# Kernel tuning notes

Measured on AMD Instinct MI355X. Metric: run time of the kernel, lower is better.

Reference implementation:

```python
import jax, jax.numpy as jnp
import numpy as np

B, H, D, S = 128, 32, 128, 64   # batch, num_head, size_per_head, seq_len
START_LEN = 32
SCALE = 0.125  # hard-coded in source (not 1/sqrt(D))


def setup_inputs() -> dict:
    key = jax.random.key(0)
    ks = jax.random.split(key, 7)
    w_std = 1.0 / np.sqrt(D)  # xavier-ish, keeps softmax well-conditioned
    return {
        "x": jax.random.normal(ks[0], (B, H, 1, D), dtype=jnp.float32),
        "k": jax.random.normal(ks[1], (B, H, S, D), dtype=jnp.float32),
        "v": jax.random.normal(ks[2], (B, H, S, D), dtype=jnp.float32),
        "weight_q": jax.random.normal(ks[3], (H, D, D), dtype=jnp.float32) * w_std,
        "weight_k": jax.random.normal(ks[4], (H, D, D), dtype=jnp.float32) * w_std,
        "weight_v": jax.random.normal(ks[5], (H, D, D), dtype=jnp.float32) * w_std,
        "weight_o": jax.random.normal(ks[6], (H, D, D), dtype=jnp.float32) * w_std,
    }


def reference(x, k, v, weight_q, weight_k, weight_v, weight_o):
    # scatters K/V into the cache at gen_id, then attends over the FULL cache
    # (including not-yet-written zero slots, exactly as the torch code does).
    def step(carry, gen_id):
        x, k, v = carry
        q = jnp.einsum('bhod,hde->bhoe', x, weight_q)          # [B,H,1,D]
        k_new = jnp.einsum('bhod,hde->bhe', x, weight_k)       # [B,H,D]
        v_new = jnp.einsum('bhod,hde->bhe', x, weight_v)
        k = jax.lax.dynamic_update_slice_in_dim(k, k_new[:, :, None, :], gen_id, axis=2)
        v = jax.lax.dynamic_update_slice_in_dim(v, v_new[:, :, None, :], gen_id, axis=2)
        attn = jnp.einsum('bhsd,bhod->bhos', k, q) * SCALE     # [B,H,1,S]
        attn = jax.nn.softmax(attn, axis=3)
        x = jnp.einsum('bhos,bhsd->bhod', attn, v)             # [B,H,1,D]
        x = jnp.einsum('bhod,hde->bhoe', x, weight_o)
        return (x, k, v), None

    (x, k, v), _ = jax.lax.scan(step, (x, k, v), jnp.arange(START_LEN, S))
    return (k, v, x)
```

## Files before the change

### kernel.cpp

```cpp
#include <hip/hip_runtime.h>
#include <math.h>

#define B 128
#define H 32
#define D 128
#define S 64
#define T0 32
#define SCALE 0.125f

#define NB 2
#define NT 512
#define KVS 132

#define OFF_KL 0
#define OFF_VL (OFF_KL + NB*S*KVS)
#define OFF_X2 (OFF_VL + NB*S*KVS)
#define OFF_QB (OFF_X2 + 256)
#define OFF_XO (OFF_QB + 256)
#define OFF_RED (OFF_XO + 256)
#define OFF_AT (OFF_RED + 4096)
#define LDS_FLOATS (OFF_AT + 128)
#define LDS_BYTES (LDS_FLOATS*4)

__global__ void __launch_bounds__(NT, 2)
attn_decode_kernel(const float* __restrict__ x_in,
                   const float* __restrict__ k_in,
                   const float* __restrict__ v_in,
                   const float* __restrict__ wq,
                   const float* __restrict__ wk,
                   const float* __restrict__ wv,
                   const float* __restrict__ wo,
                   float* __restrict__ out)
{
    extern __shared__ float smem[];
    float* Kl    = smem + OFF_KL;
    float* Vl    = smem + OFF_VL;
    float* x2    = smem + OFF_X2;
    float* qb    = smem + OFF_QB;
    float* xo2   = smem + OFF_XO;
    float* red   = smem + OFF_RED;
    float* attnp = smem + OFF_AT;

    const int tid = threadIdx.x;
    const int blk = (blockIdx.x & 7) * 256 + (blockIdx.x >> 3);
    const int h  = blk >> 6;
    const int b0 = (blk & 63) << 1;

    const int m  = tid >> 7;
    const int dq = (tid >> 5) & 3;
    const int cg = tid & 31;
    const int ds = tid >> 5;

    float4 w[32];
    if (m < 3) {
        const float* Wm = (m == 0 ? wq : (m == 1 ? wk : wv)) + h*D*D + (dq*32)*D + cg*4;
        #pragma unroll
        for (int i = 0; i < 32; ++i)
            w[i] = *reinterpret_cast<const float4*>(Wm + i*D);
    }
    float4 wob[8];
    {
        const float* Wo = wo + h*D*D + (ds*8)*D + cg*4;
        #pragma unroll
        for (int i = 0; i < 8; ++i)
            wob[i] = *reinterpret_cast<const float4*>(Wo + i*D);
    }

    for (int i = tid; i < NB*S*(D/4); i += NT) {
        int p = i >> 11, s = (i >> 5) & 63, g = i & 31;
        size_t base = (size_t)((b0+p)*H + h) * S * D;
        float4 k4 = reinterpret_cast<const float4*>(k_in + base)[s*32 + g];
        float4 v4 = reinterpret_cast<const float4*>(v_in + base)[s*32 + g];
        *reinterpret_cast<float4*>(&Kl[(p*S + s)*KVS + g*4]) = k4;
        *reinterpret_cast<float4*>(&Vl[(p*S + s)*KVS + g*4]) = v4;
    }
    if (tid < 256) {
        int p = tid >> 7, d = tid & 127;
        x2[d*2 + p] = x_in[(size_t)((b0+p)*H + h)*D + d];
    }
    __syncthreads();

    for (int t = T0; t < S; ++t) {
        if (m < 3) {
            float4 a0 = {0,0,0,0}, a1 = {0,0,0,0};
            #pragma unroll
            for (int i = 0; i < 32; ++i) {
                float2 xd = *reinterpret_cast<const float2*>(&x2[(dq*32 + i)*2]);
                a0.x = fmaf(xd.x, w[i].x, a0.x); a0.y = fmaf(xd.x, w[i].y, a0.y);
                a0.z = fmaf(xd.x, w[i].z, a0.z); a0.w = fmaf(xd.x, w[i].w, a0.w);
                a1.x = fmaf(xd.y, w[i].x, a1.x); a1.y = fmaf(xd.y, w[i].y, a1.y);
                a1.z = fmaf(xd.y, w[i].z, a1.z); a1.w = fmaf(xd.y, w[i].w, a1.w);
            }
            *reinterpret_cast<float4*>(&red[((m*4 + dq)*2 + 0)*128 + cg*4]) = a0;
            *reinterpret_cast<float4*>(&red[((m*4 + dq)*2 + 1)*128 + cg*4]) = a1;
        }
        __syncthreads();
        for (int u = tid; u < 768; u += NT) {
            int mm = u >> 8, p = (u >> 7) & 1, col = u & 127;
            float sm = red[((mm*4+0)*2+p)*128+col] + red[((mm*4+1)*2+p)*128+col]
                     + red[((mm*4+2)*2+p)*128+col] + red[((mm*4+3)*2+p)*128+col];
            if (mm == 0)      qb[p*128 + col] = sm;
            else if (mm == 1) Kl[(p*S + t)*KVS + col] = sm;
            else              Vl[(p*S + t)*KVS + col] = sm;
        }
        __syncthreads();

        {
            int p = tid >> 8, dqq = (tid >> 6) & 3, s = tid & 63;
            const float* kr = &Kl[(p*S + s)*KVS + dqq*32];
            const float* qr = &qb[p*128 + dqq*32];
            float acc = 0.f;
            #pragma unroll
            for (int j = 0; j < 8; ++j) {
                float4 kk = *reinterpret_cast<const float4*>(kr + j*4);
                float4 qq = *reinterpret_cast<const float4*>(qr + j*4);
                acc = fmaf(kk.x, qq.x, fmaf(kk.y, qq.y, fmaf(kk.z, qq.z, fmaf(kk.w, qq.w, acc))));
            }
            red[(p*4 + dqq)*64 + s] = acc;
        }
        __syncthreads();

        if (tid < 128) {
            int p = tid >> 6, s = tid & 63;
            float a = (red[(p*4+0)*64+s] + red[(p*4+1)*64+s]
                     + red[(p*4+2)*64+s] + red[(p*4+3)*64+s]) * SCALE;
            float mx = a;
            #pragma unroll
            for (int k2 = 32; k2; k2 >>= 1) mx = fmaxf(mx, __shfl_xor(mx, k2));
            float e = expf(a - mx);
            float ssum = e;
            #pragma unroll
            for (int k2 = 32; k2; k2 >>= 1) ssum += __shfl_xor(ssum, k2);
            attnp[p*64 + s] = e / ssum;
        }
        __syncthreads();

        {
            int p = tid >> 8, sh = (tid >> 7) & 1, col = tid & 127;
            const float* pp = &attnp[p*64 + sh*32];
            float acc = 0.f;
            #pragma unroll
            for (int i = 0; i < 32; ++i)
                acc = fmaf(pp[i], Vl[(p*S + sh*32 + i)*KVS + col], acc);
            red[(p*2 + sh)*128 + col] = acc;
        }
        __syncthreads();
        if (tid < 256) {
            int p = tid >> 7, col = tid & 127;
            xo2[col*2 + p] = red[(p*2+0)*128+col] + red[(p*2+1)*128+col];
        }
        __syncthreads();

        {
            float4 a0 = {0,0,0,0}, a1 = {0,0,0,0};
            #pragma unroll
            for (int i = 0; i < 8; ++i) {
                float2 xd = *reinterpret_cast<const float2*>(&xo2[(ds*8 + i)*2]);
                a0.x = fmaf(xd.x, wob[i].x, a0.x); a0.y = fmaf(xd.x, wob[i].y, a0.y);
                a0.z = fmaf(xd.x, wob[i].z, a0.z); a0.w = fmaf(xd.x, wob[i].w, a0.w);
                a1.x = fmaf(xd.y, wob[i].x, a1.x); a1.y = fmaf(xd.y, wob[i].y, a1.y);
                a1.z = fmaf(xd.y, wob[i].z, a1.z); a1.w = fmaf(xd.y, wob[i].w, a1.w);
            }
            *reinterpret_cast<float4*>(&red[(ds*2 + 0)*128 + cg*4]) = a0;
            *reinterpret_cast<float4*>(&red[(ds*2 + 1)*128 + cg*4]) = a1;
        }
        __syncthreads();
        if (tid < 256) {
            int p = tid >> 7, col = tid & 127;
            float sm = 0.f;
            #pragma unroll
            for (int d16 = 0; d16 < 16; ++d16) sm += red[(d16*2 + p)*128 + col];
            x2[col*2 + p] = sm;
        }
        __syncthreads();
    }

    float* kout = out;
    float* vout = out + (size_t)B*H*S*D;
    float* xout = out + (size_t)2*B*H*S*D;
    for (int i = tid; i < NB*S*(D/4); i += NT) {
        int p = i >> 11, s = (i >> 5) & 63, g = i & 31;
        size_t base = (size_t)((b0+p)*H + h) * S * D;
        float4 k4 = *reinterpret_cast<const float4*>(&Kl[(p*S + s)*KVS + g*4]);
        float4 v4 = *reinterpret_cast<const float4*>(&Vl[(p*S + s)*KVS + g*4]);
        reinterpret_cast<float4*>(kout + base)[s*32 + g] = k4;
        reinterpret_cast<float4*>(vout + base)[s*32 + g] = v4;
    }
    if (tid < 256) {
        int p = tid >> 7, d = tid & 127;
        xout[(size_t)((b0+p)*H + h)*D + d] = x2[d*2 + p];
    }
}

extern "C" void kernel_launch(void* const* d_in, const int* in_sizes, int n_in,
                              void* d_out, int out_size, void* d_ws, size_t ws_size,
                              hipStream_t stream) {
    (void)in_sizes; (void)n_in; (void)out_size; (void)d_ws; (void)ws_size;
    const float* x  = (const float*)d_in[0];
    const float* k  = (const float*)d_in[1];
    const float* v  = (const float*)d_in[2];
    const float* wq = (const float*)d_in[3];
    const float* wk = (const float*)d_in[4];
    const float* wv = (const float*)d_in[5];
    const float* wo = (const float*)d_in[6];
    float* out = (float*)d_out;

    hipFuncSetAttribute(reinterpret_cast<const void*>(attn_decode_kernel),
                        hipFuncAttributeMaxDynamicSharedMemorySize, LDS_BYTES);

    dim3 grid(B*H/NB);
    dim3 block(NT);
    attn_decode_kernel<<<grid, block, LDS_BYTES, stream>>>(x, k, v, wq, wk, wv, wo, out);
}
```

Measured before the change: 1.211 ms.

## Replace LDS partial-sum reductions with wave shuffles and cut per-step barriers

Each decode step is re-partitioned so that every wave computes its slice of the Q/K/V projections, the QK scores, the softmax-weighted V sum and the output projection. Partial sums are reduced with cross-lane shuffles instead of an LDS staging buffer, which removes several reduction passes and roughly halves the __syncthreads barriers per step. All threads now keep scalar slices of all four weight matrices in registers, and the q, x and xo buffers use padded LDS layouts to avoid bank conflicts. In exchange it adds heavy register pressure (128 weight floats per thread), which could spill, plus extra shuffle traffic.

```diff
diff --git a/kernel.cpp b/kernel.cpp
--- a/kernel.cpp
+++ b/kernel.cpp
@@ -12,14 +12,17 @@
 #define NT 512
 #define KVS 132
 
+#define X2IDX(d,p) ((((d)>>5)*66) + (((d)&31)<<1) + (p))
+#define QPIDX(p,d) ((p)*160 + (((d)>>4)*20) + ((d)&15))
+
+#define SZ_KV  (NB*S*KVS)
 #define OFF_KL 0
-#define OFF_VL (OFF_KL + NB*S*KVS)
-#define OFF_X2 (OFF_VL + NB*S*KVS)
-#define OFF_QB (OFF_X2 + 256)
-#define OFF_XO (OFF_QB + 256)
-#define OFF_RED (OFF_XO + 256)
-#define OFF_AT (OFF_RED + 4096)
-#define LDS_FLOATS (OFF_AT + 128)
+#define OFF_VL (OFF_KL + SZ_KV)
+#define OFF_X2 (OFF_VL + SZ_KV)
+#define OFF_QP (OFF_X2 + 264)
+#define OFF_XO (OFF_QP + 320)
+#define OFF_SC (OFF_XO + 264)
+#define LDS_FLOATS (OFF_SC + 128)
 #define LDS_BYTES (LDS_FLOATS*4)
 
 __global__ void __launch_bounds__(NT, 2)
@@ -33,37 +36,37 @@
                    float* __restrict__ out)
 {
     extern __shared__ float smem[];
-    float* Kl    = smem + OFF_KL;
-    float* Vl    = smem + OFF_VL;
-    float* x2    = smem + OFF_X2;
-    float* qb    = smem + OFF_QB;
-    float* xo2   = smem + OFF_XO;
-    float* red   = smem + OFF_RED;
-    float* attnp = smem + OFF_AT;
+    float* Kl = smem + OFF_KL;
+    float* Vl = smem + OFF_VL;
+    float* x2 = smem + OFF_X2;
+    float* qp = smem + OFF_QP;
+    float* xo = smem + OFF_XO;
+    float* sc = smem + OFF_SC;
 
     const int tid = threadIdx.x;
+    const int w = tid >> 6;
+    const int l = tid & 63;
     const int blk = (blockIdx.x & 7) * 256 + (blockIdx.x >> 3);
     const int h  = blk >> 6;
     const int b0 = (blk & 63) << 1;
 
-    const int m  = tid >> 7;
-    const int dq = (tid >> 5) & 3;
-    const int cg = tid & 31;
-    const int ds = tid >> 5;
-
-    float4 w[32];
-    if (m < 3) {
-        const float* Wm = (m == 0 ? wq : (m == 1 ? wk : wv)) + h*D*D + (dq*32)*D + cg*4;
+    const int colw = w*16 + (l & 15);
+    const int qd   = l >> 4;
+
+    float wq_r[32], wk_r[32], wv_r[32], wo_r[32];
+    {
+        const size_t wbase = (size_t)h*D*D + (size_t)(qd*32)*D + colw;
+        const float* bq = wq + wbase;
+        const float* bk = wk + wbase;
+        const float* bv = wv + wbase;
+        const float* bo = wo + wbase;
         #pragma unroll
-        for (int i = 0; i < 32; ++i)
-            w[i] = *reinterpret_cast<const float4*>(Wm + i*D);
-    }
-    float4 wob[8];
-    {
-        const float* Wo = wo + h*D*D + (ds*8)*D + cg*4;
-        #pragma unroll
-        for (int i = 0; i < 8; ++i)
-            wob[i] = *reinterpret_cast<const float4*>(Wo + i*D);
+        for (int i = 0; i < 32; ++i) {
+            wq_r[i] = bq[i*D];
+            wk_r[i] = bk[i*D];
+            wv_r[i] = bv[i*D];
+            wo_r[i] = bo[i*D];
+        }
     }
 
     for (int i = tid; i < NB*S*(D/4); i += NT) {
@@ -76,101 +79,99 @@
     }
     if (tid < 256) {
         int p = tid >> 7, d = tid & 127;
-        x2[d*2 + p] = x_in[(size_t)((b0+p)*H + h)*D + d];
+        x2[X2IDX(d,p)] = x_in[(size_t)((b0+p)*H + h)*D + d];
     }
     __syncthreads();
 
+    const int s2 = w*8 + (l & 7);
+    const int e8 = l >> 3;
+    const int p4 = w >> 2;
+    const int colb = ((w & 3) << 5) + (l & 31);
+    const int sh = l >> 5;
+
     for (int t = T0; t < S; ++t) {
-        if (m < 3) {
-            float4 a0 = {0,0,0,0}, a1 = {0,0,0,0};
+        {
+            float aq0=0.f, aq1=0.f, ak0=0.f, ak1=0.f, av0=0.f, av1=0.f;
             #pragma unroll
             for (int i = 0; i < 32; ++i) {
-                float2 xd = *reinterpret_cast<const float2*>(&x2[(dq*32 + i)*2]);
-                a0.x = fmaf(xd.x, w[i].x, a0.x); a0.y = fmaf(xd.x, w[i].y, a0.y);
-                a0.z = fmaf(xd.x, w[i].z, a0.z); a0.w = fmaf(xd.x, w[i].w, a0.w);
-                a1.x = fmaf(xd.y, w[i].x, a1.x); a1.y = fmaf(xd.y, w[i].y, a1.y);
-                a1.z = fmaf(xd.y, w[i].z, a1.z); a1.w = fmaf(xd.y, w[i].w, a1.w);
-            }
-            *reinterpret_cast<float4*>(&red[((m*4 + dq)*2 + 0)*128 + cg*4]) = a0;
-            *reinterpret_cast<float4*>(&red[((m*4 + dq)*2 + 1)*128 + cg*4]) = a1;
-        }
-        __syncthreads();
-        for (int u = tid; u < 768; u += NT) {
-            int mm = u >> 8, p = (u >> 7) & 1, col = u & 127;
-            float sm = red[((mm*4+0)*2+p)*128+col] + red[((mm*4+1)*2+p)*128+col]
-                     + red[((mm*4+2)*2+p)*128+col] + red[((mm*4+3)*2+p)*128+col];
-            if (mm == 0)      qb[p*128 + col] = sm;
-            else if (mm == 1) Kl[(p*S + t)*KVS + col] = sm;
-            else              Vl[(p*S + t)*KVS + col] = sm;
-        }
-        __syncthreads();
-
-        {
-            int p = tid >> 8, dqq = (tid >> 6) & 3, s = tid & 63;
-            const float* kr = &Kl[(p*S + s)*KVS + dqq*32];
-            const float* qr = &qb[p*128 + dqq*32];
+                float2 xv = *reinterpret_cast<const float2*>(&x2[qd*66 + (i<<1)]);
+                float wqi = wq_r[i], wki = wk_r[i], wvi = wv_r[i];
+                aq0 = fmaf(xv.x, wqi, aq0); aq1 = fmaf(xv.y, wqi, aq1);
+                ak0 = fmaf(xv.x, wki, ak0); ak1 = fmaf(xv.y, wki, ak1);
+                av0 = fmaf(xv.x, wvi, av0); av1 = fmaf(xv.y, wvi, av1);
+            }
+            aq0 += __shfl_xor(aq0,16); aq0 += __shfl_xor(aq0,32);
+            aq1 += __shfl_xor(aq1,16); aq1 += __shfl_xor(aq1,32);
+            ak0 += __shfl_xor(ak0,16); ak0 += __shfl_xor(ak0,32);
+            ak1 += __shfl_xor(ak1,16); ak1 += __shfl_xor(ak1,32);
+            av0 += __shfl_xor(av0,16); av0 += __shfl_xor(av0,32);
+            av1 += __shfl_xor(av1,16); av1 += __shfl_xor(av1,32);
+            if (l < 16) {
+                qp[QPIDX(0,colw)] = aq0 * SCALE;
+                qp[QPIDX(1,colw)] = aq1 * SCALE;
+                Kl[(0*S + t)*KVS + colw] = ak0;
+                Kl[(1*S + t)*KVS + colw] = ak1;
+                Vl[(0*S + t)*KVS + colw] = av0;
+                Vl[(1*S + t)*KVS + colw] = av1;
+            }
+        }
+        __syncthreads();
+
+        {
+            float sA = 0.f, sB = 0.f;
+            #pragma unroll
+            for (int j = 0; j < 4; ++j) {
+                float4 q0 = *reinterpret_cast<const float4*>(&qp[0*160 + e8*20 + j*4]);
+                float4 k0 = *reinterpret_cast<const float4*>(&Kl[(0*S + s2)*KVS + e8*16 + j*4]);
+                sA = fmaf(q0.x,k0.x, fmaf(q0.y,k0.y, fmaf(q0.z,k0.z, fmaf(q0.w,k0.w, sA))));
+                float4 q1 = *reinterpret_cast<const float4*>(&qp[1*160 + e8*20 + j*4]);
+                float4 k1 = *reinterpret_cast<const float4*>(&Kl[(1*S + s2)*KVS + e8*16 + j*4]);
+                sB = fmaf(q1.x,k1.x, fmaf(q1.y,k1.y, fmaf(q1.z,k1.z, fmaf(q1.w,k1.w, sB))));
+            }
+            sA += __shfl_xor(sA,8); sA += __shfl_xor(sA,16); sA += __shfl_xor(sA,32);
+            sB += __shfl_xor(sB,8); sB += __shfl_xor(sB,16); sB += __shfl_xor(sB,32);
+            if (l < 8) {
+                float2 scv; scv.x = sA; scv.y = sB;
+                *reinterpret_cast<float2*>(&sc[s2 << 1]) = scv;
+            }
+        }
+        __syncthreads();
+
+        {
+            float a = sc[(l << 1) + p4];
+            float mx = a;
+            #pragma unroll
+            for (int msk = 1; msk < 64; msk <<= 1) mx = fmaxf(mx, __shfl_xor(mx, msk));
+            float e = expf(a - mx);
+            float Z = e;
+            #pragma unroll
+            for (int msk = 1; msk < 64; msk <<= 1) Z += __shfl_xor(Z, msk);
             float acc = 0.f;
-            #pragma unroll
-            for (int j = 0; j < 8; ++j) {
-                float4 kk = *reinterpret_cast<const float4*>(kr + j*4);
-                float4 qq = *reinterpret_cast<const float4*>(qr + j*4);
-                acc = fmaf(kk.x, qq.x, fmaf(kk.y, qq.y, fmaf(kk.z, qq.z, fmaf(kk.w, qq.w, acc))));
-            }
-            red[(p*4 + dqq)*64 + s] = acc;
-        }
-        __syncthreads();
-
-        if (tid < 128) {
-            int p = tid >> 6, s = tid & 63;
-            float a = (red[(p*4+0)*64+s] + red[(p*4+1)*64+s]
-                     + red[(p*4+2)*64+s] + red[(p*4+3)*64+s]) * SCALE;
-            float mx = a;
-            #pragma unroll
-            for (int k2 = 32; k2; k2 >>= 1) mx = fmaxf(mx, __shfl_xor(mx, k2));
-            float e = expf(a - mx);
-            float ssum = e;
-            #pragma unroll
-            for (int k2 = 32; k2; k2 >>= 1) ssum += __shfl_xor(ssum, k2);
-            attnp[p*64 + s] = e / ssum;
-        }
-        __syncthreads();
-
-        {
-            int p = tid >> 8, sh = (tid >> 7) & 1, col = tid & 127;
-            const float* pp = &attnp[p*64 + sh*32];
-            float acc = 0.f;
-            #pragma unroll
-            for (int i = 0; i < 32; ++i)
-                acc = fmaf(pp[i], Vl[(p*S + sh*32 + i)*KVS + col], acc);
-            red[(p*2 + sh)*128 + col] = acc;
-        }
-        __syncthreads();
-        if (tid < 256) {
-            int p = tid >> 7, col = tid & 127;
-            xo2[col*2 + p] = red[(p*2+0)*128+col] + red[(p*2+1)*128+col];
-        }
-        __syncthreads();
-
-        {
-            float4 a0 = {0,0,0,0}, a1 = {0,0,0,0};
-            #pragma unroll
-            for (int i = 0; i < 8; ++i) {
-                float2 xd = *reinterpret_cast<const float2*>(&xo2[(ds*8 + i)*2]);
-                a0.x = fmaf(xd.x, wob[i].x, a0.x); a0.y = fmaf(xd.x, wob[i].y, a0.y);
-                a0.z = fmaf(xd.x, wob[i].z, a0.z); a0.w = fmaf(xd.x, wob[i].w, a0.w);
-                a1.x = fmaf(xd.y, wob[i].x, a1.x); a1.y = fmaf(xd.y, wob[i].y, a1.y);
-                a1.z = fmaf(xd.y, wob[i].z, a1.z); a1.w = fmaf(xd.y, wob[i].w, a1.w);
-            }
-            *reinterpret_cast<float4*>(&red[(ds*2 + 0)*128 + cg*4]) = a0;
-            *reinterpret_cast<float4*>(&red[(ds*2 + 1)*128 + cg*4]) = a1;
-        }
-        __syncthreads();
-        if (tid < 256) {
-            int p = tid >> 7, col = tid & 127;
-            float sm = 0.f;
-            #pragma unroll
-            for (int d16 = 0; d16 < 16; ++d16) sm += red[(d16*2 + p)*128 + col];
-            x2[col*2 + p] = sm;
+            const float* Vrow = &Vl[(p4*S + (sh<<5))*KVS + colb];
+            #pragma unroll
+            for (int i = 0; i < 32; ++i) {
+                float es = __shfl(e, (sh<<5) + i);
+                acc = fmaf(es, Vrow[i*KVS], acc);
+            }
+            acc += __shfl_xor(acc, 32);
+            if (l < 32) xo[X2IDX(colb, p4)] = acc / Z;
+        }
+        __syncthreads();
+
+        {
+            float o0 = 0.f, o1 = 0.f;
+            #pragma unroll
+            for (int i = 0; i < 32; ++i) {
+                float2 xv = *reinterpret_cast<const float2*>(&xo[qd*66 + (i<<1)]);
+                o0 = fmaf(xv.x, wo_r[i], o0);
+                o1 = fmaf(xv.y, wo_r[i], o1);
+            }
+            o0 += __shfl_xor(o0,16); o0 += __shfl_xor(o0,32);
+            o1 += __shfl_xor(o1,16); o1 += __shfl_xor(o1,32);
+            if (l < 16) {
+                float2 xn; xn.x = o0; xn.y = o1;
+                *reinterpret_cast<float2*>(&x2[((colw>>5)*66) + ((colw&31)<<1)]) = xn;
+            }
         }
         __syncthreads();
     }
@@ -188,7 +189,7 @@
     }
     if (tid < 256) {
         int p = tid >> 7, d = tid & 127;
-        xout[(size_t)((b0+p)*H + h)*D + d] = x2[d*2 + p];
+        xout[(size_t)((b0+p)*H + h)*D + d] = x2[X2IDX(d,p)];
     }
 }
 
```

Measured after the change: 1.358 ms. +12.2%, slower.
